# Kernel tuning notes

Measured on AMD Instinct MI355X. Metric: run time of the kernel, lower is better.

Reference implementation:

```python
import jax, jax.numpy as jnp
import numpy as np
import math

B, D = 32768, 64

def setup_inputs() -> dict:
    key = jax.random.key(0)
    k1, k2, k3 = jax.random.split(key, 3)
    x = jax.random.normal(k1, (B, D), dtype=jnp.float32)
    grad_H = jax.random.normal(k2, (B, D), dtype=jnp.float32)
    # kaiming-normal-like init: std = sqrt(2 / fan_in), fan_in = D+1
    weight = jax.random.normal(k3, (D + 1, D * D), dtype=jnp.float32) * np.float32(math.sqrt(2.0 / (D + 1)))
    return {"x": x, "grad_H": grad_H, "weight": weight}

def reference(x, grad_H, weight):
    b, d = x.shape
    x1 = jnp.concatenate([x, jnp.ones((b, 1), dtype=x.dtype)], axis=1)  # (B, D+1)
    M = (x1 @ weight).reshape(b, d, d)                                   # (B, D, D)
    R = jnp.einsum('bik,bjk->bij', M, M) / jnp.asarray(math.sqrt(d), x.dtype)  # M @ M^T
    return jnp.einsum('bd,bde->be', grad_H, R)                           # (B, D)
```

## Files before the change

kernel.cpp:

```cpp
#include <hip/hip_runtime.h>
#include <stdint.h>

typedef _Float16  f16;
typedef f16       f16x2  __attribute__((ext_vector_type(2)));
typedef f16       f16x8  __attribute__((ext_vector_type(8)));
typedef float     f32x16v __attribute__((ext_vector_type(16)));
typedef float     f32x4v  __attribute__((ext_vector_type(4)));
typedef uint32_t  u32x4v  __attribute__((ext_vector_type(4)));
typedef unsigned short u16;

__device__ __forceinline__ f32x16v mfma16h(u32x4v a, u32x4v b, f32x16v c) {
  return __builtin_amdgcn_mfma_f32_32x32x16_f16(
      __builtin_bit_cast(f16x8, a), __builtin_bit_cast(f16x8, b), c, 0, 0, 0);
}

__global__ __launch_bounds__(256) void prep_w(const float* __restrict__ W,
                                              u16* __restrict__ w1h,
                                              u16* __restrict__ w2h) {
  __shared__ float Wl[4096];
  const int jj = blockIdx.x;
  const int t  = threadIdx.x;
  for (int idx = t; idx < 4096; idx += 256) Wl[idx] = W[jj * 4096 + idx];
  __syncthreads();
  for (int pq = t; pq < 512; pq += 256) {
    const int c2 = pq >> 6, l = pq & 63;
    const int ct = c2 >> 2, s = c2 & 3;
    const int rowA = ct * 32 + (l & 31);
    const int k0   = s * 16 + (l >> 5) * 8;
    u16 v1[8], v2[8];
    #pragma unroll
    for (int e = 0; e < 8; ++e) {
      v2[e] = __builtin_bit_cast(u16, (f16)Wl[rowA * 64 + k0 + e]);
      v1[e] = __builtin_bit_cast(u16, (f16)Wl[(k0 + e) * 64 + rowA]);
    }
    u32x4v pk1, pk2;
    #pragma unroll
    for (int q = 0; q < 4; ++q) {
      pk1[q] = (uint32_t)v1[2*q] | ((uint32_t)v1[2*q+1] << 16);
      pk2[q] = (uint32_t)v2[2*q] | ((uint32_t)v2[2*q+1] << 16);
    }
    *reinterpret_cast<u32x4v*>(w1h + jj * 4096 + pq * 8) = pk1;
    *reinterpret_cast<u32x4v*>(w2h + jj * 4096 + pq * 8) = pk2;
  }
}

__global__ __launch_bounds__(512, 2) void rquad_main(
    const float* __restrict__ x, const float* __restrict__ g,
    const u16* __restrict__ w1h, const u16* __restrict__ w2h,
    float* __restrict__ out) {
  __shared__ u16      stage[4][8192];
  __shared__ float    vl[128 * 68];
  __shared__ uint32_t x1p[65 * 64];

  const int t    = threadIdx.x;
  const int lane = t & 63;
  const int wv   = t >> 6;
  const int jq   = wv >> 2;
  const int p    = (wv >> 1) & 1;
  const int ct   = wv & 1;
  const int bl   = lane & 31;
  const int half = lane >> 5;
  const long base = (long)blockIdx.x * 128;
  const int r0 = p * 64 + bl, r1 = r0 + 32;

  for (int q = t; q < 2048; q += 512) {
    const int row = q >> 4, c4 = (q & 15) * 4;
    *reinterpret_cast<f32x4v*>(&vl[row * 68 + c4]) =
        *reinterpret_cast<const f32x4v*>(&x[(base + row) * 64 + c4]);
  }
  __syncthreads();
  for (int idx = t; idx < 65 * 64; idx += 512) {
    const int j = idx >> 6, q = idx & 63, pp = q >> 5, qq = q & 31;
    uint32_t val;
    if (j == 64) val = 0x3C003C00u;
    else {
      f16 a = (f16)vl[(pp * 64 + qq) * 68 + j];
      f16 b = (f16)vl[(pp * 64 + 32 + qq) * 68 + j];
      val = (uint32_t)__builtin_bit_cast(u16, a) |
            ((uint32_t)__builtin_bit_cast(u16, b) << 16);
    }
    x1p[idx] = val;
  }

  f16x2 z0[4][4], z1[4][4];
  #pragma unroll
  for (int s = 0; s < 4; ++s) {
    const float* gp0 = g + (base + r0) * 64 + s * 16 + half * 8;
    const float* gp1 = g + (base + r1) * 64 + s * 16 + half * 8;
    f32x4v a = *reinterpret_cast<const f32x4v*>(gp0);
    f32x4v b = *reinterpret_cast<const f32x4v*>(gp0 + 4);
    f32x4v c = *reinterpret_cast<const f32x4v*>(gp1);
    f32x4v d = *reinterpret_cast<const f32x4v*>(gp1 + 4);
    z0[s][0] = f16x2{(f16)a[0],(f16)a[1]}; z0[s][1] = f16x2{(f16)a[2],(f16)a[3]};
    z0[s][2] = f16x2{(f16)b[0],(f16)b[1]}; z0[s][3] = f16x2{(f16)b[2],(f16)b[3]};
    z1[s][0] = f16x2{(f16)c[0],(f16)c[1]}; z1[s][1] = f16x2{(f16)c[2],(f16)c[3]};
    z1[s][2] = f16x2{(f16)d[0],(f16)d[1]}; z1[s][3] = f16x2{(f16)d[2],(f16)d[3]};
  }

  f32x16v acc0, acc1;

  auto stage_chunk = [&](const u16* __restrict__ Wsrc, int ci) {
    const int nch = (jq == 0) ? 9 : 8;
    if (ci >= nch) return;
    const int j0  = (jq == 0) ? ci * 4 : 33 + ci * 4;
    const int njs = (jq == 0 && ci == 8) ? 1 : 4;
    const int buf = jq * 2 + (ci & 1);
    #pragma unroll
    for (int u = 0; u < 2; ++u) {
      const int jl = 2 * p + u;
      if (jl < njs) {
        #pragma unroll
        for (int s = 0; s < 2; ++s) {
          const u16* src = Wsrc + (size_t)(j0 + jl) * 4096 + ct * 2048 + s * 512 + lane * 8;
          __builtin_amdgcn_global_load_lds(
              (const __attribute__((address_space(1))) void*)src,
              (__attribute__((address_space(3))) void*)(
                  &stage[buf][jl * 2048 + ct * 1024 + s * 512 + lane * 8]),
              16, 0, 0);
        }
      }
    }
  };

  auto compute_j = [&](const u16* __restrict__ Wsrc, int buf, int jl, int jglob) {
    const u16* gp = Wsrc + (size_t)jglob * 4096 + ct * 2048 + 1024 + lane * 8;
    u32x4v B2 = *reinterpret_cast<const u32x4v*>(gp);
    u32x4v B3 = *reinterpret_cast<const u32x4v*>(gp + 512);
    const u16* sb = &stage[buf][jl * 2048 + ct * 1024 + lane * 8];
    u32x4v B0 = *reinterpret_cast<const u32x4v*>(sb);
    u32x4v B1 = *reinterpret_cast<const u32x4v*>(sb + 512);
    const uint32_t xw = x1p[jglob * 64 + p * 32 + bl];
    const f16 xlo = __builtin_bit_cast(f16, (u16)(xw & 0xffffu));
    const f16 xhi = __builtin_bit_cast(f16, (u16)(xw >> 16));
    const f16x2 xx0 = f16x2{xlo, xlo}, xx1 = f16x2{xhi, xhi};
    u32x4v Bs[4] = {B0, B1, B2, B3};
    #pragma unroll
    for (int s = 0; s < 4; ++s) {
      u32x4v a0, a1;
      #pragma unroll
      for (int q = 0; q < 4; ++q) {
        a0[q] = __builtin_bit_cast(uint32_t, f16x2(xx0 * z0[s][q]));
        a1[q] = __builtin_bit_cast(uint32_t, f16x2(xx1 * z1[s][q]));
      }
      acc0 = mfma16h(a0, Bs[s], acc0);
      acc1 = mfma16h(a1, Bs[s], acc1);
    }
  };

  auto run_pass = [&](const u16* __restrict__ Wsrc) {
    #pragma unroll
    for (int r = 0; r < 16; ++r) { acc0[r] = 0.0f; acc1[r] = 0.0f; }
    stage_chunk(Wsrc, 0);
    __syncthreads();
    for (int st = 0; st < 9; ++st) {
      stage_chunk(Wsrc, st + 1);
      const int buf = jq * 2 + (st & 1);
      if (st < 8) {
        const int jbase = (jq == 0) ? st * 4 : 33 + st * 4;
        #pragma unroll
        for (int jl = 0; jl < 4; ++jl) compute_j(Wsrc, buf, jl, jbase + jl);
      } else if (jq == 0) {
        compute_j(Wsrc, buf, 0, 32);
      }
      __syncthreads();
    }
  };

  run_pass(w1h);

  if (jq == 0) {
    #pragma unroll
    for (int r = 0; r < 16; ++r) {
      const int rr = (r & 3) + 8 * (r >> 2) + 4 * half;
      vl[(p * 64 + rr) * 68 + ct * 32 + bl]      = acc0[r];
      vl[(p * 64 + 32 + rr) * 68 + ct * 32 + bl] = acc1[r];
    }
  }
  __syncthreads();
  if (jq == 1) {
    #pragma unroll
    for (int r = 0; r < 16; ++r) {
      const int rr = (r & 3) + 8 * (r >> 2) + 4 * half;
      vl[(p * 64 + rr) * 68 + ct * 32 + bl]      += acc0[r];
      vl[(p * 64 + 32 + rr) * 68 + ct * 32 + bl] += acc1[r];
    }
  }
  __syncthreads();
  #pragma unroll
  for (int s = 0; s < 4; ++s) {
    const float* vp0 = &vl[r0 * 68 + s * 16 + half * 8];
    const float* vp1 = &vl[r1 * 68 + s * 16 + half * 8];
    f32x4v a = *reinterpret_cast<const f32x4v*>(vp0);
    f32x4v b = *reinterpret_cast<const f32x4v*>(vp0 + 4);
    f32x4v c = *reinterpret_cast<const f32x4v*>(vp1);
    f32x4v d = *reinterpret_cast<const f32x4v*>(vp1 + 4);
    z0[s][0] = f16x2{(f16)a[0],(f16)a[1]}; z0[s][1] = f16x2{(f16)a[2],(f16)a[3]};
    z0[s][2] = f16x2{(f16)b[0],(f16)b[1]}; z0[s][3] = f16x2{(f16)b[2],(f16)b[3]};
    z1[s][0] = f16x2{(f16)c[0],(f16)c[1]}; z1[s][1] = f16x2{(f16)c[2],(f16)c[3]};
    z1[s][2] = f16x2{(f16)d[0],(f16)d[1]}; z1[s][3] = f16x2{(f16)d[2],(f16)d[3]};
  }

  run_pass(w2h);

  if (jq == 0) {
    #pragma unroll
    for (int r = 0; r < 16; ++r) {
      const int rr = (r & 3) + 8 * (r >> 2) + 4 * half;
      vl[(p * 64 + rr) * 68 + ct * 32 + bl]      = acc0[r];
      vl[(p * 64 + 32 + rr) * 68 + ct * 32 + bl] = acc1[r];
    }
  }
  __syncthreads();
  if (jq == 1) {
    #pragma unroll
    for (int r = 0; r < 16; ++r) {
      const int rr = (r & 3) + 8 * (r >> 2) + 4 * half;
      vl[(p * 64 + rr) * 68 + ct * 32 + bl]      += acc0[r];
      vl[(p * 64 + 32 + rr) * 68 + ct * 32 + bl] += acc1[r];
    }
  }
  __syncthreads();
  for (int q = t; q < 2048; q += 512) {
    const int row = q >> 4, c4 = (q & 15) * 4;
    f32x4v v4 = *reinterpret_cast<const f32x4v*>(&vl[row * 68 + c4]);
    f32x4v o;
    o[0] = v4[0] * 0.125f; o[1] = v4[1] * 0.125f;
    o[2] = v4[2] * 0.125f; o[3] = v4[3] * 0.125f;
    *reinterpret_cast<f32x4v*>(&out[(base + row) * 64 + c4]) = o;
  }
}

extern "C" void kernel_launch(void* const* d_in, const int* in_sizes, int n_in,
                              void* d_out, int out_size, void* d_ws, size_t ws_size,
                              hipStream_t stream) {
  const float* x = (const float*)d_in[0];
  const float* g = (const float*)d_in[1];
  const float* W = (const float*)d_in[2];
  float* o = (float*)d_out;
  u16* w1h = (u16*)d_ws;
  u16* w2h = w1h + 65 * 4096;
  hipLaunchKernelGGL(prep_w, dim3(65), dim3(256), 0, stream, W, w1h, w2h);
  hipLaunchKernelGGL(rquad_main, dim3(256), dim3(512), 0, stream, x, g, w1h, w2h, o);
}
```

Before: 52.31 us.

## Repartition waves over K-slices with triple-buffered W staging and vmcnt pipelining

```diff
diff --git a/kernel.cpp b/kernel.cpp
--- a/kernel.cpp
+++ b/kernel.cpp
@@ -48,20 +48,18 @@
     const float* __restrict__ x, const float* __restrict__ g,
     const u16* __restrict__ w1h, const u16* __restrict__ w2h,
     float* __restrict__ out) {
-  __shared__ u16      stage[4][8192];
+  __shared__ u16      stage[3 * 16384];
   __shared__ float    vl[128 * 68];
   __shared__ uint32_t x1p[65 * 64];
 
   const int t    = threadIdx.x;
   const int lane = t & 63;
   const int wv   = t >> 6;
-  const int jq   = wv >> 2;
-  const int p    = (wv >> 1) & 1;
-  const int ct   = wv & 1;
+  const int ct   = wv >> 2;
+  const int sq   = wv & 3;
   const int bl   = lane & 31;
   const int half = lane >> 5;
   const long base = (long)blockIdx.x * 128;
-  const int r0 = p * 64 + bl, r1 = r0 + 32;
 
   for (int q = t; q < 2048; q += 512) {
     const int row = q >> 4, c4 = (q & 15) * 4;
@@ -70,155 +68,127 @@
   }
   __syncthreads();
   for (int idx = t; idx < 65 * 64; idx += 512) {
-    const int j = idx >> 6, q = idx & 63, pp = q >> 5, qq = q & 31;
+    const int j = idx >> 6, q = idx & 63;
     uint32_t val;
     if (j == 64) val = 0x3C003C00u;
     else {
-      f16 a = (f16)vl[(pp * 64 + qq) * 68 + j];
-      f16 b = (f16)vl[(pp * 64 + 32 + qq) * 68 + j];
+      f16 a = (f16)vl[q * 68 + j];
+      f16 b = (f16)vl[(64 + q) * 68 + j];
       val = (uint32_t)__builtin_bit_cast(u16, a) |
             ((uint32_t)__builtin_bit_cast(u16, b) << 16);
     }
     x1p[idx] = val;
   }
-
-  f16x2 z0[4][4], z1[4][4];
-  #pragma unroll
-  for (int s = 0; s < 4; ++s) {
-    const float* gp0 = g + (base + r0) * 64 + s * 16 + half * 8;
-    const float* gp1 = g + (base + r1) * 64 + s * 16 + half * 8;
-    f32x4v a = *reinterpret_cast<const f32x4v*>(gp0);
-    f32x4v b = *reinterpret_cast<const f32x4v*>(gp0 + 4);
-    f32x4v c = *reinterpret_cast<const f32x4v*>(gp1);
-    f32x4v d = *reinterpret_cast<const f32x4v*>(gp1 + 4);
-    z0[s][0] = f16x2{(f16)a[0],(f16)a[1]}; z0[s][1] = f16x2{(f16)a[2],(f16)a[3]};
-    z0[s][2] = f16x2{(f16)b[0],(f16)b[1]}; z0[s][3] = f16x2{(f16)b[2],(f16)b[3]};
-    z1[s][0] = f16x2{(f16)c[0],(f16)c[1]}; z1[s][1] = f16x2{(f16)c[2],(f16)c[3]};
-    z1[s][2] = f16x2{(f16)d[0],(f16)d[1]}; z1[s][3] = f16x2{(f16)d[2],(f16)d[3]};
-  }
-
-  f32x16v acc0, acc1;
-
-  auto stage_chunk = [&](const u16* __restrict__ Wsrc, int ci) {
-    const int nch = (jq == 0) ? 9 : 8;
-    if (ci >= nch) return;
-    const int j0  = (jq == 0) ? ci * 4 : 33 + ci * 4;
-    const int njs = (jq == 0 && ci == 8) ? 1 : 4;
-    const int buf = jq * 2 + (ci & 1);
-    #pragma unroll
-    for (int u = 0; u < 2; ++u) {
-      const int jl = 2 * p + u;
-      if (jl < njs) {
-        #pragma unroll
-        for (int s = 0; s < 2; ++s) {
-          const u16* src = Wsrc + (size_t)(j0 + jl) * 4096 + ct * 2048 + s * 512 + lane * 8;
-          __builtin_amdgcn_global_load_lds(
-              (const __attribute__((address_space(1))) void*)src,
-              (__attribute__((address_space(3))) void*)(
-                  &stage[buf][jl * 2048 + ct * 1024 + s * 512 + lane * 8]),
-              16, 0, 0);
-        }
-      }
-    }
+  f16x2 z[4][4];
+  #pragma unroll
+  for (int tt = 0; tt < 4; ++tt) {
+    const float* gp = g + (base + tt * 32 + bl) * 64 + sq * 16 + half * 8;
+    f32x4v a = *reinterpret_cast<const f32x4v*>(gp);
+    f32x4v b = *reinterpret_cast<const f32x4v*>(gp + 4);
+    z[tt][0] = f16x2{(f16)a[0], (f16)a[1]};
+    z[tt][1] = f16x2{(f16)a[2], (f16)a[3]};
+    z[tt][2] = f16x2{(f16)b[0], (f16)b[1]};
+    z[tt][3] = f16x2{(f16)b[2], (f16)b[3]};
+  }
+  __syncthreads();
+  for (int idx = t; idx < 128 * 68; idx += 512) vl[idx] = 0.0f;
+  __syncthreads();
+
+  f32x16v acc[4];
+  const int fragoff = ct * 2048 + sq * 512;
+
+  auto stage_chunk = [&](const u16* __restrict__ Wsrc, int c) {
+    if (c > 16) return;
+    const int nu = (c == 16) ? 1 : 4;
+    u16* dstb = &stage[(c % 3) * 16384 + fragoff];
+    const u16* srcb = Wsrc + (size_t)c * 4 * 4096 + fragoff + lane * 8;
+    for (int u = 0; u < nu; ++u)
+      __builtin_amdgcn_global_load_lds(
+          (const __attribute__((address_space(1))) void*)(srcb + (size_t)u * 4096),
+          (__attribute__((address_space(3))) void*)(dstb + u * 4096),
+          16, 0, 0);
   };
 
-  auto compute_j = [&](const u16* __restrict__ Wsrc, int buf, int jl, int jglob) {
-    const u16* gp = Wsrc + (size_t)jglob * 4096 + ct * 2048 + 1024 + lane * 8;
-    u32x4v B2 = *reinterpret_cast<const u32x4v*>(gp);
-    u32x4v B3 = *reinterpret_cast<const u32x4v*>(gp + 512);
-    const u16* sb = &stage[buf][jl * 2048 + ct * 1024 + lane * 8];
-    u32x4v B0 = *reinterpret_cast<const u32x4v*>(sb);
-    u32x4v B1 = *reinterpret_cast<const u32x4v*>(sb + 512);
-    const uint32_t xw = x1p[jglob * 64 + p * 32 + bl];
-    const f16 xlo = __builtin_bit_cast(f16, (u16)(xw & 0xffffu));
-    const f16 xhi = __builtin_bit_cast(f16, (u16)(xw >> 16));
-    const f16x2 xx0 = f16x2{xlo, xlo}, xx1 = f16x2{xhi, xhi};
-    u32x4v Bs[4] = {B0, B1, B2, B3};
-    #pragma unroll
-    for (int s = 0; s < 4; ++s) {
-      u32x4v a0, a1;
+  auto compute_chunk = [&](int st) {
+    const int nj = (st == 16) ? 1 : 4;
+    const u16* sb = &stage[(st % 3) * 16384 + fragoff + lane * 8];
+    for (int jl = 0; jl < nj; ++jl) {
+      const int jglob = st * 4 + jl;
+      u32x4v B = *reinterpret_cast<const u32x4v*>(sb + jl * 4096);
+      const uint32_t xw0 = x1p[jglob * 64 + bl];
+      const uint32_t xw1 = x1p[jglob * 64 + 32 + bl];
+      const f16x2 xp0 = __builtin_bit_cast(f16x2, xw0);
+      const f16x2 xp1 = __builtin_bit_cast(f16x2, xw1);
+      const f16x2 xb0 = f16x2{xp0[0], xp0[0]};
+      const f16x2 xb1 = f16x2{xp1[0], xp1[0]};
+      const f16x2 xb2 = f16x2{xp0[1], xp0[1]};
+      const f16x2 xb3 = f16x2{xp1[1], xp1[1]};
+      u32x4v a0, a1, a2, a3;
       #pragma unroll
       for (int q = 0; q < 4; ++q) {
-        a0[q] = __builtin_bit_cast(uint32_t, f16x2(xx0 * z0[s][q]));
-        a1[q] = __builtin_bit_cast(uint32_t, f16x2(xx1 * z1[s][q]));
+        a0[q] = __builtin_bit_cast(uint32_t, f16x2(xb0 * z[0][q]));
+        a1[q] = __builtin_bit_cast(uint32_t, f16x2(xb1 * z[1][q]));
+        a2[q] = __builtin_bit_cast(uint32_t, f16x2(xb2 * z[2][q]));
+        a3[q] = __builtin_bit_cast(uint32_t, f16x2(xb3 * z[3][q]));
       }
-      acc0 = mfma16h(a0, Bs[s], acc0);
-      acc1 = mfma16h(a1, Bs[s], acc1);
+      acc[0] = mfma16h(a0, B, acc[0]);
+      acc[1] = mfma16h(a1, B, acc[1]);
+      acc[2] = mfma16h(a2, B, acc[2]);
+      acc[3] = mfma16h(a3, B, acc[3]);
     }
   };
 
   auto run_pass = [&](const u16* __restrict__ Wsrc) {
     #pragma unroll
-    for (int r = 0; r < 16; ++r) { acc0[r] = 0.0f; acc1[r] = 0.0f; }
+    for (int tt = 0; tt < 4; ++tt)
+      #pragma unroll
+      for (int r = 0; r < 16; ++r) acc[tt][r] = 0.0f;
     stage_chunk(Wsrc, 0);
-    __syncthreads();
-    for (int st = 0; st < 9; ++st) {
-      stage_chunk(Wsrc, st + 1);
-      const int buf = jq * 2 + (st & 1);
-      if (st < 8) {
-        const int jbase = (jq == 0) ? st * 4 : 33 + st * 4;
-        #pragma unroll
-        for (int jl = 0; jl < 4; ++jl) compute_j(Wsrc, buf, jl, jbase + jl);
-      } else if (jq == 0) {
-        compute_j(Wsrc, buf, 0, 32);
-      }
-      __syncthreads();
+    stage_chunk(Wsrc, 1);
+    stage_chunk(Wsrc, 2);
+    for (int st = 0; st <= 16; ++st) {
+      if (st < 14)       asm volatile("s_waitcnt vmcnt(8)" ::: "memory");
+      else if (st == 14) asm volatile("s_waitcnt vmcnt(5)" ::: "memory");
+      else if (st == 15) asm volatile("s_waitcnt vmcnt(1)" ::: "memory");
+      else               asm volatile("s_waitcnt vmcnt(0)" ::: "memory");
+      __builtin_amdgcn_sched_barrier(0);
+      compute_chunk(st);
+      __builtin_amdgcn_sched_barrier(0);
+      stage_chunk(Wsrc, st + 3);
     }
   };
 
   run_pass(w1h);
-
-  if (jq == 0) {
+  #pragma unroll
+  for (int tt = 0; tt < 4; ++tt)
     #pragma unroll
     for (int r = 0; r < 16; ++r) {
       const int rr = (r & 3) + 8 * (r >> 2) + 4 * half;
-      vl[(p * 64 + rr) * 68 + ct * 32 + bl]      = acc0[r];
-      vl[(p * 64 + 32 + rr) * 68 + ct * 32 + bl] = acc1[r];
-    }
-  }
-  __syncthreads();
-  if (jq == 1) {
+      atomicAdd(&vl[(tt * 32 + rr) * 68 + ct * 32 + bl], acc[tt][r]);
+    }
+  __syncthreads();
+  #pragma unroll
+  for (int tt = 0; tt < 4; ++tt) {
+    const float* vp = &vl[(tt * 32 + bl) * 68 + sq * 16 + half * 8];
+    f32x4v a = *reinterpret_cast<const f32x4v*>(vp);
+    f32x4v b = *reinterpret_cast<const f32x4v*>(vp + 4);
+    z[tt][0] = f16x2{(f16)a[0], (f16)a[1]};
+    z[tt][1] = f16x2{(f16)a[2], (f16)a[3]};
+    z[tt][2] = f16x2{(f16)b[0], (f16)b[1]};
+    z[tt][3] = f16x2{(f16)b[2], (f16)b[3]};
+  }
+  __syncthreads();
+  for (int idx = t; idx < 128 * 68; idx += 512) vl[idx] = 0.0f;
+  __syncthreads();
+
+  run_pass(w2h);
+  #pragma unroll
+  for (int tt = 0; tt < 4; ++tt)
     #pragma unroll
     for (int r = 0; r < 16; ++r) {
       const int rr = (r & 3) + 8 * (r >> 2) + 4 * half;
-      vl[(p * 64 + rr) * 68 + ct * 32 + bl]      += acc0[r];
-      vl[(p * 64 + 32 + rr) * 68 + ct * 32 + bl] += acc1[r];
-    }
-  }
-  __syncthreads();
-  #pragma unroll
-  for (int s = 0; s < 4; ++s) {
-    const float* vp0 = &vl[r0 * 68 + s * 16 + half * 8];
-    const float* vp1 = &vl[r1 * 68 + s * 16 + half * 8];
-    f32x4v a = *reinterpret_cast<const f32x4v*>(vp0);
-    f32x4v b = *reinterpret_cast<const f32x4v*>(vp0 + 4);
-    f32x4v c = *reinterpret_cast<const f32x4v*>(vp1);
-    f32x4v d = *reinterpret_cast<const f32x4v*>(vp1 + 4);
-    z0[s][0] = f16x2{(f16)a[0],(f16)a[1]}; z0[s][1] = f16x2{(f16)a[2],(f16)a[3]};
-    z0[s][2] = f16x2{(f16)b[0],(f16)b[1]}; z0[s][3] = f16x2{(f16)b[2],(f16)b[3]};
-    z1[s][0] = f16x2{(f16)c[0],(f16)c[1]}; z1[s][1] = f16x2{(f16)c[2],(f16)c[3]};
-    z1[s][2] = f16x2{(f16)d[0],(f16)d[1]}; z1[s][3] = f16x2{(f16)d[2],(f16)d[3]};
-  }
-
-  run_pass(w2h);
-
-  if (jq == 0) {
-    #pragma unroll
-    for (int r = 0; r < 16; ++r) {
-      const int rr = (r & 3) + 8 * (r >> 2) + 4 * half;
-      vl[(p * 64 + rr) * 68 + ct * 32 + bl]      = acc0[r];
-      vl[(p * 64 + 32 + rr) * 68 + ct * 32 + bl] = acc1[r];
-    }
-  }
-  __syncthreads();
-  if (jq == 1) {
-    #pragma unroll
-    for (int r = 0; r < 16; ++r) {
-      const int rr = (r & 3) + 8 * (r >> 2) + 4 * half;
-      vl[(p * 64 + rr) * 68 + ct * 32 + bl]      += acc0[r];
-      vl[(p * 64 + 32 + rr) * 68 + ct * 32 + bl] += acc1[r];
-    }
-  }
+      atomicAdd(&vl[(tt * 32 + rr) * 68 + ct * 32 + bl], acc[tt][r]);
+    }
   __syncthreads();
   for (int q = t; q < 2048; q += 512) {
     const int row = q >> 4, c4 = (q & 15) * 4;
```

Measured after the change: 131.8 us. 152% more time.
